# Kernel tuning notes

Hardware: AMD Instinct MI355X
Metric: run time of the kernel (lower is better)

The kernel has to match this reference:

```python
import jax, jax.numpy as jnp
import numpy as np

B, S, D = 2, 2048, 1024
H, DH = 16, 64
N_CTX = 2048
IGNORE = -100000.0


def setup_inputs() -> dict:
    key = jax.random.key(0)
    ks = jax.random.split(key, 6)
    scale = 0.02
    return {
        "x": jax.random.normal(ks[0], (B, S, D), dtype=jnp.float32),
        "W_Q": jax.random.normal(ks[1], (H, DH, D), dtype=jnp.float32) * scale,
        "W_K": jax.random.normal(ks[2], (H, DH, D), dtype=jnp.float32) * scale,
        "W_V": jax.random.normal(ks[3], (H, DH, D), dtype=jnp.float32) * scale,
        "W_O": jax.random.normal(ks[4], (H, D, DH), dtype=jnp.float32) * scale,
        "b_Q": jnp.zeros((H, DH), dtype=jnp.float32),
        "b_K": jnp.zeros((H, DH), dtype=jnp.float32),
        "b_V": jnp.zeros((H, DH), dtype=jnp.float32),
        "b_O": jnp.zeros((D,), dtype=jnp.float32),
    }


def reference(x, W_Q, W_K, W_V, W_O, b_Q, b_K, b_V, b_O):
    attn_scale = jnp.sqrt(jnp.asarray(DH, dtype=x.dtype))
    # q,k,v: [batch, pos, head, d_head]
    q = jnp.einsum('ihm,bpm->bpih', W_Q, x) + b_Q
    k = jnp.einsum('ihm,bpm->bpih', W_K, x) + b_K
    v = jnp.einsum('ihm,bpm->bpih', W_V, x) + b_V
    # scores: [batch, head, q_pos, k_pos]
    attn_scores = jnp.einsum('bpih,bqih->bipq', q, k) / attn_scale
    # causal mask (pos_start=0, no kv cache)
    qs, ks_ = attn_scores.shape[-2], attn_scores.shape[-1]
    mask = jnp.tril(jnp.ones((qs, ks_), dtype=bool))
    attn_scores = jnp.where(mask, attn_scores, jnp.asarray(IGNORE, dtype=attn_scores.dtype))
    attn_matrix = jax.nn.softmax(attn_scores, axis=-1)
    # z: [batch, q_pos, head, d_head]
    z = jnp.einsum('bpih,biqp->bqih', v, attn_matrix)
    out = jnp.einsum('idh,bqih->bqd', W_O, z) + b_O
    return out
```

## Files before the change

### kernel.cpp

```cpp
#include <hip/hip_runtime.h>

typedef __bf16 bf16;
typedef __bf16 bf16x4 __attribute__((ext_vector_type(4)));
typedef __bf16 bf16x8 __attribute__((ext_vector_type(8)));
typedef float f32x4 __attribute__((ext_vector_type(4)));
typedef unsigned u32x4 __attribute__((ext_vector_type(4)));
typedef unsigned u32x2 __attribute__((ext_vector_type(2)));

#define AS1C(p) ((const __attribute__((address_space(1))) void*)(p))
#define AS3(p)  ((__attribute__((address_space(3))) void*)(p))

__device__ __forceinline__ void gld16(const bf16* gsrc, bf16* ldst) {
  __builtin_amdgcn_global_load_lds(AS1C(gsrc), AS3(ldst), 16, 0, 0);
}

#define QSCALE 0.18033688011112042f

__global__ void prep_all(const float* __restrict__ x,
                         const float* __restrict__ WQ, const float* __restrict__ WK,
                         const float* __restrict__ WV, const float* __restrict__ WO,
                         const float* __restrict__ bQ, const float* __restrict__ bK,
                         const float* __restrict__ bV,
                         bf16* __restrict__ xb, bf16* __restrict__ Wqkv,
                         bf16* __restrict__ Wo2, float* __restrict__ biasq) {
  const int X4 = (4096 * 1024) / 4;
  const int WN = 1024 * 1024;
  const int total = X4 + 4 * WN + 3072;
  for (int i = blockIdx.x * blockDim.x + threadIdx.x; i < total; i += gridDim.x * blockDim.x) {
    if (i < X4) {
      float4 v = ((const float4*)x)[i];
      bf16x4 o;
      o[0] = (bf16)v.x; o[1] = (bf16)v.y; o[2] = (bf16)v.z; o[3] = (bf16)v.w;
      ((bf16x4*)xb)[i] = o;
    } else {
      int j = i - X4;
      if (j < WN) {
        Wqkv[j] = (bf16)(WQ[j] * QSCALE);
      } else if (j < 2 * WN) {
        Wqkv[j] = (bf16)WK[j - WN];
      } else if (j < 3 * WN) {
        Wqkv[j] = (bf16)WV[j - 2 * WN];
      } else if (j < 4 * WN) {
        int k = j - 3 * WN;
        int hh = k >> 16, r = k & 65535, d = r >> 6, dh = r & 63;
        Wo2[d * 1024 + hh * 64 + dh] = (bf16)WO[k];
      } else {
        int n = j - 4 * WN;
        biasq[n] = (n < 1024) ? bQ[n] * QSCALE : (n < 2048) ? bK[n - 1024] : bV[n - 2048];
      }
    }
  }
}

template <int MODE>
__global__ __launch_bounds__(256, 2)
void gemm_bt(const bf16* __restrict__ A, const bf16* __restrict__ Bw,
             const float* __restrict__ bias,
             bf16* __restrict__ Qo, bf16* __restrict__ Ko, bf16* __restrict__ Vt,
             float* __restrict__ Co, int M, int N, int K) {
  __shared__ bf16 As[2][8192];
  __shared__ bf16 Bs[2][8192];
  const int tid = threadIdx.x;
  const int lane = tid & 63, w = tid >> 6;
  const int wr = w >> 1, wc = w & 1;
  const int g = lane >> 4, lr = lane & 15;
  const int perx = gridDim.x >> 3;
  const int tile = (blockIdx.x & 7) * perx + (blockIdx.x >> 3);
  const int brow = (tile & 31) * 128, bcol = (tile >> 5) * 128;

  auto stage = [&](int k0, int bufi) {
#pragma unroll
    for (int it = 0; it < 4; ++it) {
      const int cb = (it * 4 + w) * 64;
      const int u = cb + lane;
      const int lc = u ^ ((u >> 3) & 7);
      const int row = lc >> 3, c8 = (lc & 7) * 8;
      gld16(A + (size_t)(brow + row) * K + k0 + c8, &As[bufi][cb * 8]);
      gld16(Bw + (size_t)(bcol + row) * K + k0 + c8, &Bs[bufi][cb * 8]);
    }
  };

  f32x4 acc[4][4] = {};
  stage(0, 0);
  const int nstep = K >> 6;

  for (int t = 0; t < nstep; ++t) {
    __syncthreads();
    if (t + 1 < nstep) stage((t + 1) << 6, (t + 1) & 1);
    const bf16* as = As[t & 1];
    const bf16* bs = Bs[t & 1];
#pragma unroll
    for (int kk = 0; kk < 2; ++kk) {
      bf16x8 af[4], bfm[4];
#pragma unroll
      for (int m = 0; m < 4; ++m) {
        const int row = wr * 64 + m * 16 + lr;
        const int sl = (row * 8 + kk * 4 + g) ^ (lr & 7);
        af[m] = *(const bf16x8*)(as + sl * 8);
      }
#pragma unroll
      for (int n = 0; n < 4; ++n) {
        const int row = wc * 64 + n * 16 + lr;
        const int sl = (row * 8 + kk * 4 + g) ^ (lr & 7);
        bfm[n] = *(const bf16x8*)(bs + sl * 8);
      }
#pragma unroll
      for (int m = 0; m < 4; ++m)
#pragma unroll
        for (int n = 0; n < 4; ++n)
          acc[m][n] = __builtin_amdgcn_mfma_f32_16x16x32_bf16(af[m], bfm[n], acc[m][n], 0, 0, 0);
    }
  }

  const int row0 = brow + wr * 64;
  const int col0 = bcol + wc * 64;
#pragma unroll
  for (int m = 0; m < 4; ++m) {
#pragma unroll
    for (int n = 0; n < 4; ++n) {
      const int nidx = col0 + n * 16 + lr;
      f32x4 v = acc[m][n];
      const float bs = bias[nidx];
      if (MODE == 0) {
        const int stream = nidx >> 10;
        const int j = nidx & 1023;
        const int hh = j >> 6, dh = j & 63;
        const int r0 = row0 + m * 16 + g * 4;
        const int b = r0 >> 11;
        const int p0 = r0 & 2047;
        if (stream == 2) {
          bf16x4 vv;
#pragma unroll
          for (int i = 0; i < 4; ++i) vv[i] = (bf16)(v[i] + bs);
          *(bf16x4*)(Vt + ((size_t)(b * 16 + hh) * 64 + dh) * 2048 + p0) = vv;
        } else {
          bf16* dst = (stream == 0) ? Qo : Ko;
#pragma unroll
          for (int i = 0; i < 4; ++i)
            dst[((size_t)(b * 16 + hh) * 2048 + (p0 + i)) * 64 + dh] = (bf16)(v[i] + bs);
        }
      } else {
#pragma unroll
        for (int i = 0; i < 4; ++i) {
          const int r = row0 + m * 16 + g * 4 + i;
          Co[(size_t)r * 1024 + nidx] = v[i] + bs;
        }
      }
    }
  }
}

__global__ __launch_bounds__(256, 4)
void attn_kernel(const bf16* __restrict__ Qm, const bf16* __restrict__ Km,
                 const bf16* __restrict__ Vm, bf16* __restrict__ Z,
                 bf16* __restrict__ OP, float2* __restrict__ ML) {
  const int nblk = blockIdx.x;
  const int xcd = nblk & 7, s2 = nblk >> 3;
  const int Gl = s2 & 3, u = s2 >> 2;
  const int G = Gl * 8 + xcd;
  const int hh = G & 15, b = G >> 4;
  const int lane = threadIdx.x & 63, w = threadIdx.x >> 6;
  const int g = lane >> 4, lr = lane & 15;
  const bool g0 = g & 1, g1 = (g >> 1) & 1;

  int qt, t0, t1, spl;
  if (u < 32) {
    qt = 31 - (u >> 1); spl = u & 1;
    const int T = qt + 1, mid = (T + 1) >> 1;
    t0 = spl ? mid : 0; t1 = spl ? T : mid;
  } else {
    qt = 47 - u; spl = -1; t0 = 0; t1 = qt + 1;
  }

  __shared__ bf16 Ks[2][4096];
  __shared__ bf16 Vs[2][4096];

  const bf16* Qb = Qm + (size_t)G * 2048 * 64;
  const bf16* Kb = Km + (size_t)G * 2048 * 64;
  const bf16* Vb = Vm + (size_t)G * 64 * 2048;

  auto stage = [&](int kv0, int bufi) {
#pragma unroll
    for (int it = 0; it < 2; ++it) {
      const int cb = w * 128 + it * 64;
      const int uu = cb + lane;
      const int lc = uu ^ ((uu >> 3) & 7);
      const int row = lc >> 3, c8 = (lc & 7) * 8;
      gld16(Kb + (size_t)(kv0 + row) * 64 + c8, &Ks[bufi][cb * 8]);
      gld16(Vb + (size_t)row * 2048 + kv0 + c8, &Vs[bufi][cb * 8]);
    }
  };

  const int q0w = qt * 64 + w * 16;
  const int qg = q0w + lr;

  bf16x8 aq[2];
#pragma unroll
  for (int kk = 0; kk < 2; ++kk)
    aq[kk] = *(const bf16x8*)(Qb + (size_t)qg * 64 + kk * 32 + g * 8);

  float m_i = -1e30f, l_i = 0.f;
  f32x4 oacc[4] = {};

  int buf = 0;
  stage(t0 * 64, 0);
  __syncthreads();

  for (int t = t0; t < t1; ++t) {
    if (t + 1 < t1) stage((t + 1) * 64, buf ^ 1);
    const int kv0 = t * 64;

    f32x4 s[4] = {};
#pragma unroll
    for (int kk = 0; kk < 2; ++kk) {
#pragma unroll
      for (int n = 0; n < 4; ++n) {
        const int r = n * 16 + lr;
        const int sl = (r * 8 + kk * 4 + g) ^ (r & 7);
        bf16x8 bk = *(const bf16x8*)(&Ks[buf][sl * 8]);
        s[n] = __builtin_amdgcn_mfma_f32_16x16x32_bf16(bk, aq[kk], s[n], 0, 0, 0);
      }
    }
    if (t == qt) {
#pragma unroll
      for (int n = 0; n < 4; ++n)
#pragma unroll
        for (int i = 0; i < 4; ++i)
          if (kv0 + n * 16 + g * 4 + i > qg) s[n][i] = -1e9f;
    }

    float tm = fmaxf(fmaxf(fmaxf(s[0][0], s[0][1]), fmaxf(s[0][2], s[0][3])),
                     fmaxf(fmaxf(s[1][0], s[1][1]), fmaxf(s[1][2], s[1][3])));
    tm = fmaxf(tm, fmaxf(fmaxf(fmaxf(s[2][0], s[2][1]), fmaxf(s[2][2], s[2][3])),
                         fmaxf(fmaxf(s[3][0], s[3][1]), fmaxf(s[3][2], s[3][3]))));
    tm = fmaxf(tm, __shfl_xor(tm, 16));
    tm = fmaxf(tm, __shfl_xor(tm, 32));
    if (!__all(tm <= m_i + 12.f)) {
      const float mn = fmaxf(m_i, tm);
      const float al = exp2f(m_i - mn);
      m_i = mn;
      l_i *= al;
#pragma unroll
      for (int n = 0; n < 4; ++n)
#pragma unroll
        for (int i = 0; i < 4; ++i) oacc[n][i] *= al;
    }
#pragma unroll
    for (int n = 0; n < 4; ++n)
#pragma unroll
      for (int i = 0; i < 4; ++i) s[n][i] = exp2f(s[n][i] - m_i);
    float ts = ((s[0][0] + s[0][1]) + (s[0][2] + s[0][3])) +
               ((s[1][0] + s[1][1]) + (s[1][2] + s[1][3])) +
               ((s[2][0] + s[2][1]) + (s[2][2] + s[2][3])) +
               ((s[3][0] + s[3][1]) + (s[3][2] + s[3][3]));
    ts += __shfl_xor(ts, 16);
    ts += __shfl_xor(ts, 32);
    l_i += ts;

    unsigned U[8];
#pragma unroll
    for (int n = 0; n < 4; ++n)
#pragma unroll
      for (int h = 0; h < 2; ++h) {
        unsigned lo = (unsigned)__builtin_bit_cast(unsigned short, (bf16)s[n][2 * h]);
        unsigned hi = (unsigned)__builtin_bit_cast(unsigned short, (bf16)s[n][2 * h + 1]);
        U[n * 2 + h] = lo | (hi << 16);
      }
    unsigned v2_000, v2_001, v2_010, v2_011, v2_100, v2_101, v2_110, v2_111;
#if __has_builtin(__builtin_amdgcn_permlane32_swap)
    {
      u32x2 pA0 = __builtin_amdgcn_permlane32_swap(U[0], U[2], false, false);
      u32x2 pA1 = __builtin_amdgcn_permlane32_swap(U[1], U[3], false, false);
      u32x2 pA2 = __builtin_amdgcn_permlane32_swap(U[4], U[6], false, false);
      u32x2 pA3 = __builtin_amdgcn_permlane32_swap(U[5], U[7], false, false);
      v2_000 = pA0[0]; v2_010 = pA0[1];
      v2_001 = pA1[0]; v2_011 = pA1[1];
      v2_100 = pA2[0]; v2_110 = pA2[1];
      v2_101 = pA3[0]; v2_111 = pA3[1];
    }
#else
    {
      unsigned rA0 = (unsigned)__shfl_xor((int)(g1 ? U[0] : U[2]), 32);
      unsigned rA1 = (unsigned)__shfl_xor((int)(g1 ? U[1] : U[3]), 32);
      unsigned rA2 = (unsigned)__shfl_xor((int)(g1 ? U[4] : U[6]), 32);
      unsigned rA3 = (unsigned)__shfl_xor((int)(g1 ? U[5] : U[7]), 32);
      v2_000 = g1 ? rA0 : U[0];
      v2_001 = g1 ? rA1 : U[1];
      v2_010 = g1 ? U[2] : rA0;
      v2_011 = g1 ? U[3] : rA1;
      v2_100 = g1 ? rA2 : U[4];
      v2_101 = g1 ? rA3 : U[5];
      v2_110 = g1 ? U[6] : rA2;
      v2_111 = g1 ? U[7] : rA3;
    }
#endif
    u32x4 t0v, t1v;
#if __has_builtin(__builtin_amdgcn_permlane16_swap)
    {
      u32x2 pB0 = __builtin_amdgcn_permlane16_swap(v2_000, v2_010, false, false);
      u32x2 pB1 = __builtin_amdgcn_permlane16_swap(v2_001, v2_011, false, false);
      u32x2 pB2 = __builtin_amdgcn_permlane16_swap(v2_100, v2_110, false, false);
      u32x2 pB3 = __builtin_amdgcn_permlane16_swap(v2_101, v2_111, false, false);
      t0v[0] = pB0[0]; t0v[2] = pB0[1];
      t0v[1] = pB1[0]; t0v[3] = pB1[1];
      t1v[0] = pB2[0]; t1v[2] = pB2[1];
      t1v[1] = pB3[0]; t1v[3] = pB3[1];
    }
#else
    {
      unsigned rB0 = (unsigned)__shfl_xor((int)(g0 ? v2_000 : v2_010), 16);
      unsigned rB1 = (unsigned)__shfl_xor((int)(g0 ? v2_001 : v2_011), 16);
      unsigned rB2 = (unsigned)__shfl_xor((int)(g0 ? v2_100 : v2_110), 16);
      unsigned rB3 = (unsigned)__shfl_xor((int)(g0 ? v2_101 : v2_111), 16);
      t0v[0] = g0 ? rB0 : v2_000;
      t0v[1] = g0 ? rB1 : v2_001;
      t0v[2] = g0 ? v2_010 : rB0;
      t0v[3] = g0 ? v2_011 : rB1;
      t1v[0] = g0 ? rB2 : v2_100;
      t1v[1] = g0 ? rB3 : v2_101;
      t1v[2] = g0 ? v2_110 : rB2;
      t1v[3] = g0 ? v2_111 : rB3;
    }
#endif
    bf16x8 pb0 = __builtin_bit_cast(bf16x8, t0v);
    bf16x8 pb1 = __builtin_bit_cast(bf16x8, t1v);

#pragma unroll
    for (int kk = 0; kk < 2; ++kk) {
      const bf16x8 pb = kk ? pb1 : pb0;
#pragma unroll
      for (int n = 0; n < 4; ++n) {
        const int r = n * 16 + lr;
        const int sl = (r * 8 + kk * 4 + g) ^ (r & 7);
        bf16x8 av = *(const bf16x8*)(&Vs[buf][sl * 8]);
        oacc[n] = __builtin_amdgcn_mfma_f32_16x16x32_bf16(av, pb, oacc[n], 0, 0, 0);
      }
    }
    __syncthreads();
    buf ^= 1;
  }

  if (u < 32) {
    const int pr = G * 1024 + (qt - 16) * 64 + w * 16 + lr;
    bf16* oprow = OP + (size_t)(spl * 32768 + pr) * 64;
#pragma unroll
    for (int n = 0; n < 4; ++n) {
      bf16x4 o4;
#pragma unroll
      for (int i = 0; i < 4; ++i) o4[i] = (bf16)oacc[n][i];
      *(bf16x4*)(oprow + n * 16 + g * 4) = o4;
    }
    if (lane < 16) ML[spl * 32768 + pr] = make_float2(m_i, l_i);
  } else {
    const float li = 1.f / l_i;
    bf16* zrow = Z + ((size_t)(b * 2048 + qg) * 16 + hh) * 64;
#pragma unroll
    for (int n = 0; n < 4; ++n) {
      bf16x4 o4;
#pragma unroll
      for (int i = 0; i < 4; ++i) o4[i] = (bf16)(oacc[n][i] * li);
      *(bf16x4*)(zrow + n * 16 + g * 4) = o4;
    }
  }
}

__global__ __launch_bounds__(256)
void combine_kernel(const bf16* __restrict__ OP, const float2* __restrict__ ML,
                    bf16* __restrict__ Z) {
  const int id = blockIdx.x * 256 + threadIdx.x;
  const int pr = id >> 3, d8 = id & 7;
  const float2 ml0 = ML[pr], ml1 = ML[32768 + pr];
  const float m = fmaxf(ml0.x, ml1.x);
  const float w0 = exp2f(ml0.x - m), w1 = exp2f(ml1.x - m);
  const float inv = 1.f / (ml0.y * w0 + ml1.y * w1);
  const bf16x8 a = *(const bf16x8*)(OP + (size_t)pr * 64 + d8 * 8);
  const bf16x8 c = *(const bf16x8*)(OP + ((size_t)32768 + pr) * 64 + d8 * 8);
  bf16x8 o;
#pragma unroll
  for (int j = 0; j < 8; ++j)
    o[j] = (bf16)(((float)a[j] * w0 + (float)c[j] * w1) * inv);
  const int bh = pr >> 10, qr = pr & 1023;
  const int bb = bh >> 4, hq = bh & 15;
  *(bf16x8*)(Z + (((size_t)(bb * 2048 + 1024 + qr)) * 16 + hq) * 64 + d8 * 8) = o;
}

extern "C" void kernel_launch(void* const* d_in, const int* in_sizes, int n_in,
                              void* d_out, int out_size, void* d_ws, size_t ws_size,
                              hipStream_t stream) {
  const float* x  = (const float*)d_in[0];
  const float* WQ = (const float*)d_in[1];
  const float* WK = (const float*)d_in[2];
  const float* WV = (const float*)d_in[3];
  const float* WO = (const float*)d_in[4];
  const float* bQ = (const float*)d_in[5];
  const float* bK = (const float*)d_in[6];
  const float* bV = (const float*)d_in[7];
  const float* bO = (const float*)d_in[8];
  float* out = (float*)d_out;

  char* ws = (char*)d_ws;
  bf16* xb    = (bf16*)(ws);
  bf16* Wqkv  = (bf16*)(ws + (8u << 20));
  bf16* Wo2   = (bf16*)(ws + (14u << 20));
  bf16* Qb    = (bf16*)(ws + (16u << 20));
  bf16* Kb    = (bf16*)(ws + (24u << 20));
  bf16* Vtb   = (bf16*)(ws + (32u << 20));
  bf16* Zb    = (bf16*)(ws + (40u << 20));
  float* biasq = (float*)(ws + (48u << 20));
  bf16* OP    = (bf16*)(ws);
  float2* ML  = (float2*)(ws + (8u << 20));

  prep_all<<<2048, 256, 0, stream>>>(x, WQ, WK, WV, WO, bQ, bK, bV, xb, Wqkv, Wo2, biasq);
  gemm_bt<0><<<768, 256, 0, stream>>>(xb, Wqkv, biasq, Qb, Kb, Vtb, nullptr,
                                      4096, 3072, 1024);
  attn_kernel<<<1536, 256, 0, stream>>>(Qb, Kb, Vtb, Zb, OP, ML);
  combine_kernel<<<1024, 256, 0, stream>>>(OP, ML, Zb);
  gemm_bt<1><<<256, 256, 0, stream>>>(Zb, Wo2, bO, nullptr, nullptr, nullptr, out,
                                      4096, 1024, 1024);
}
```

Before: 205.8 us.

## Process two 64-row query chunks per attention block to reuse K/V tiles

Each attention block now handles 128 query rows as two 64-row chunks that share every staged K/V tile in LDS. This halves K/V global loads and LDS staging per query, and halves the grid from 1536 to 768 blocks with the split and work-order scheme adjusted. In exchange, register use roughly doubles for accumulators and scores, so the occupancy hint drops from 4 to 3 blocks per CU. Diagonal masking now covers two KV tiles per block, so the upper chunk does some fully masked work.

```diff
diff --git a/kernel.cpp b/kernel.cpp
--- a/kernel.cpp
+++ b/kernel.cpp
@@ -150,7 +150,7 @@
   }
 }
 
-__global__ __launch_bounds__(256, 4)
+__global__ __launch_bounds__(256, 3)
 void attn_kernel(const bf16* __restrict__ Qm, const bf16* __restrict__ Km,
                  const bf16* __restrict__ Vm, bf16* __restrict__ Z,
                  bf16* __restrict__ OP, float2* __restrict__ ML) {
@@ -162,14 +162,16 @@
   const int lane = threadIdx.x & 63, w = threadIdx.x >> 6;
   const int g = lane >> 4, lr = lane & 15;
   const bool g0 = g & 1, g1 = (g >> 1) & 1;
-
-  int qt, t0, t1, spl;
-  if (u < 32) {
-    qt = 31 - (u >> 1); spl = u & 1;
-    const int T = qt + 1, mid = (T + 1) >> 1;
-    t0 = spl ? mid : 0; t1 = spl ? T : mid;
+  (void)g0; (void)g1;
+
+  int jt, t0, t1, spl;
+  if (u < 16) {
+    jt = 15 - (u >> 1); spl = u & 1;
+    const int mid = jt + 1;
+    t0 = spl ? mid : 0;
+    t1 = spl ? 2 * jt + 2 : mid;
   } else {
-    qt = 47 - u; spl = -1; t0 = 0; t1 = qt + 1;
+    jt = 23 - u; spl = -1; t0 = 0; t1 = 2 * jt + 2;
   }
 
   __shared__ bf16 Ks[2][4096];
@@ -191,16 +193,17 @@
     }
   };
 
-  const int q0w = qt * 64 + w * 16;
-  const int qg = q0w + lr;
-
-  bf16x8 aq[2];
-#pragma unroll
-  for (int kk = 0; kk < 2; ++kk)
-    aq[kk] = *(const bf16x8*)(Qb + (size_t)qg * 64 + kk * 32 + g * 8);
-
-  float m_i = -1e30f, l_i = 0.f;
-  f32x4 oacc[4] = {};
+  const int qr0 = jt * 128 + w * 16 + lr;
+
+  bf16x8 aq[2][2];
+#pragma unroll
+  for (int c = 0; c < 2; ++c)
+#pragma unroll
+    for (int kk = 0; kk < 2; ++kk)
+      aq[c][kk] = *(const bf16x8*)(Qb + (size_t)(qr0 + c * 64) * 64 + kk * 32 + g * 8);
+
+  float m_i[2] = {-1e30f, -1e30f}, l_i[2] = {0.f, 0.f};
+  f32x4 oacc[2][4] = {};
 
   int buf = 0;
   stage(t0 * 64, 0);
@@ -209,8 +212,9 @@
   for (int t = t0; t < t1; ++t) {
     if (t + 1 < t1) stage((t + 1) * 64, buf ^ 1);
     const int kv0 = t * 64;
-
-    f32x4 s[4] = {};
+    const bool diag = (t >= 2 * jt);
+
+    f32x4 s[2][4] = {};
 #pragma unroll
     for (int kk = 0; kk < 2; ++kk) {
 #pragma unroll
@@ -218,148 +222,166 @@
         const int r = n * 16 + lr;
         const int sl = (r * 8 + kk * 4 + g) ^ (r & 7);
         bf16x8 bk = *(const bf16x8*)(&Ks[buf][sl * 8]);
-        s[n] = __builtin_amdgcn_mfma_f32_16x16x32_bf16(bk, aq[kk], s[n], 0, 0, 0);
-      }
-    }
-    if (t == qt) {
+        s[0][n] = __builtin_amdgcn_mfma_f32_16x16x32_bf16(bk, aq[0][kk], s[0][n], 0, 0, 0);
+        s[1][n] = __builtin_amdgcn_mfma_f32_16x16x32_bf16(bk, aq[1][kk], s[1][n], 0, 0, 0);
+      }
+    }
+    if (diag) {
+#pragma unroll
+      for (int c = 0; c < 2; ++c) {
+        const int qg = qr0 + c * 64;
+#pragma unroll
+        for (int n = 0; n < 4; ++n)
+#pragma unroll
+          for (int i = 0; i < 4; ++i)
+            if (kv0 + n * 16 + g * 4 + i > qg) s[c][n][i] = -1e9f;
+      }
+    }
+
+    bf16x8 pb[2][2];
+#pragma unroll
+    for (int c = 0; c < 2; ++c) {
+      float tm = fmaxf(fmaxf(fmaxf(s[c][0][0], s[c][0][1]), fmaxf(s[c][0][2], s[c][0][3])),
+                       fmaxf(fmaxf(s[c][1][0], s[c][1][1]), fmaxf(s[c][1][2], s[c][1][3])));
+      tm = fmaxf(tm, fmaxf(fmaxf(fmaxf(s[c][2][0], s[c][2][1]), fmaxf(s[c][2][2], s[c][2][3])),
+                           fmaxf(fmaxf(s[c][3][0], s[c][3][1]), fmaxf(s[c][3][2], s[c][3][3]))));
+      tm = fmaxf(tm, __shfl_xor(tm, 16));
+      tm = fmaxf(tm, __shfl_xor(tm, 32));
+      if (!__all(tm <= m_i[c] + 12.f)) {
+        const float mn = fmaxf(m_i[c], tm);
+        const float al = exp2f(m_i[c] - mn);
+        m_i[c] = mn;
+        l_i[c] *= al;
+#pragma unroll
+        for (int n = 0; n < 4; ++n)
+#pragma unroll
+          for (int i = 0; i < 4; ++i) oacc[c][n][i] *= al;
+      }
 #pragma unroll
       for (int n = 0; n < 4; ++n)
 #pragma unroll
-        for (int i = 0; i < 4; ++i)
-          if (kv0 + n * 16 + g * 4 + i > qg) s[n][i] = -1e9f;
-    }
-
-    float tm = fmaxf(fmaxf(fmaxf(s[0][0], s[0][1]), fmaxf(s[0][2], s[0][3])),
-                     fmaxf(fmaxf(s[1][0], s[1][1]), fmaxf(s[1][2], s[1][3])));
-    tm = fmaxf(tm, fmaxf(fmaxf(fmaxf(s[2][0], s[2][1]), fmaxf(s[2][2], s[2][3])),
-                         fmaxf(fmaxf(s[3][0], s[3][1]), fmaxf(s[3][2], s[3][3]))));
-    tm = fmaxf(tm, __shfl_xor(tm, 16));
-    tm = fmaxf(tm, __shfl_xor(tm, 32));
-    if (!__all(tm <= m_i + 12.f)) {
-      const float mn = fmaxf(m_i, tm);
-      const float al = exp2f(m_i - mn);
-      m_i = mn;
-      l_i *= al;
+        for (int i = 0; i < 4; ++i) s[c][n][i] = exp2f(s[c][n][i] - m_i[c]);
+      float ts = ((s[c][0][0] + s[c][0][1]) + (s[c][0][2] + s[c][0][3])) +
+                 ((s[c][1][0] + s[c][1][1]) + (s[c][1][2] + s[c][1][3])) +
+                 ((s[c][2][0] + s[c][2][1]) + (s[c][2][2] + s[c][2][3])) +
+                 ((s[c][3][0] + s[c][3][1]) + (s[c][3][2] + s[c][3][3]));
+      ts += __shfl_xor(ts, 16);
+      ts += __shfl_xor(ts, 32);
+      l_i[c] += ts;
+
+      unsigned U[8];
 #pragma unroll
       for (int n = 0; n < 4; ++n)
 #pragma unroll
-        for (int i = 0; i < 4; ++i) oacc[n][i] *= al;
-    }
-#pragma unroll
-    for (int n = 0; n < 4; ++n)
-#pragma unroll
-      for (int i = 0; i < 4; ++i) s[n][i] = exp2f(s[n][i] - m_i);
-    float ts = ((s[0][0] + s[0][1]) + (s[0][2] + s[0][3])) +
-               ((s[1][0] + s[1][1]) + (s[1][2] + s[1][3])) +
-               ((s[2][0] + s[2][1]) + (s[2][2] + s[2][3])) +
-               ((s[3][0] + s[3][1]) + (s[3][2] + s[3][3]));
-    ts += __shfl_xor(ts, 16);
-    ts += __shfl_xor(ts, 32);
-    l_i += ts;
-
-    unsigned U[8];
-#pragma unroll
-    for (int n = 0; n < 4; ++n)
-#pragma unroll
-      for (int h = 0; h < 2; ++h) {
-        unsigned lo = (unsigned)__builtin_bit_cast(unsigned short, (bf16)s[n][2 * h]);
-        unsigned hi = (unsigned)__builtin_bit_cast(unsigned short, (bf16)s[n][2 * h + 1]);
-        U[n * 2 + h] = lo | (hi << 16);
-      }
-    unsigned v2_000, v2_001, v2_010, v2_011, v2_100, v2_101, v2_110, v2_111;
+        for (int h = 0; h < 2; ++h) {
+          unsigned lo = (unsigned)__builtin_bit_cast(unsigned short, (bf16)s[c][n][2 * h]);
+          unsigned hi = (unsigned)__builtin_bit_cast(unsigned short, (bf16)s[c][n][2 * h + 1]);
+          U[n * 2 + h] = lo | (hi << 16);
+        }
+      unsigned v2_000, v2_001, v2_010, v2_011, v2_100, v2_101, v2_110, v2_111;
 #if __has_builtin(__builtin_amdgcn_permlane32_swap)
-    {
-      u32x2 pA0 = __builtin_amdgcn_permlane32_swap(U[0], U[2], false, false);
-      u32x2 pA1 = __builtin_amdgcn_permlane32_swap(U[1], U[3], false, false);
-      u32x2 pA2 = __builtin_amdgcn_permlane32_swap(U[4], U[6], false, false);
-      u32x2 pA3 = __builtin_amdgcn_permlane32_swap(U[5], U[7], false, false);
-      v2_000 = pA0[0]; v2_010 = pA0[1];
-      v2_001 = pA1[0]; v2_011 = pA1[1];
-      v2_100 = pA2[0]; v2_110 = pA2[1];
-      v2_101 = pA3[0]; v2_111 = pA3[1];
-    }
+      {
+        u32x2 pA0 = __builtin_amdgcn_permlane32_swap(U[0], U[2], false, false);
+        u32x2 pA1 = __builtin_amdgcn_permlane32_swap(U[1], U[3], false, false);
+        u32x2 pA2 = __builtin_amdgcn_permlane32_swap(U[4], U[6], false, false);
+        u32x2 pA3 = __builtin_amdgcn_permlane32_swap(U[5], U[7], false, false);
+        v2_000 = pA0[0]; v2_010 = pA0[1];
+        v2_001 = pA1[0]; v2_011 = pA1[1];
+        v2_100 = pA2[0]; v2_110 = pA2[1];
+        v2_101 = pA3[0]; v2_111 = pA3[1];
+      }
 #else
-    {
-      unsigned rA0 = (unsigned)__shfl_xor((int)(g1 ? U[0] : U[2]), 32);
-      unsigned rA1 = (unsigned)__shfl_xor((int)(g1 ? U[1] : U[3]), 32);
-      unsigned rA2 = (unsigned)__shfl_xor((int)(g1 ? U[4] : U[6]), 32);
-      unsigned rA3 = (unsigned)__shfl_xor((int)(g1 ? U[5] : U[7]), 32);
-      v2_000 = g1 ? rA0 : U[0];
-      v2_001 = g1 ? rA1 : U[1];
-      v2_010 = g1 ? U[2] : rA0;
-      v2_011 = g1 ? U[3] : rA1;
-      v2_100 = g1 ? rA2 : U[4];
-      v2_101 = g1 ? rA3 : U[5];
-      v2_110 = g1 ? U[6] : rA2;
-      v2_111 = g1 ? U[7] : rA3;
-    }
+      {
+        const bool G1 = (lane >> 5) & 1;
+        unsigned rA0 = (unsigned)__shfl_xor((int)(G1 ? U[0] : U[2]), 32);
+        unsigned rA1 = (unsigned)__shfl_xor((int)(G1 ? U[1] : U[3]), 32);
+        unsigned rA2 = (unsigned)__shfl_xor((int)(G1 ? U[4] : U[6]), 32);
+        unsigned rA3 = (unsigned)__shfl_xor((int)(G1 ? U[5] : U[7]), 32);
+        v2_000 = G1 ? rA0 : U[0];
+        v2_001 = G1 ? rA1 : U[1];
+        v2_010 = G1 ? U[2] : rA0;
+        v2_011 = G1 ? U[3] : rA1;
+        v2_100 = G1 ? rA2 : U[4];
+        v2_101 = G1 ? rA3 : U[5];
+        v2_110 = G1 ? U[6] : rA2;
+        v2_111 = G1 ? U[7] : rA3;
+      }
 #endif
-    u32x4 t0v, t1v;
+      u32x4 t0v, t1v;
 #if __has_builtin(__builtin_amdgcn_permlane16_swap)
-    {
-      u32x2 pB0 = __builtin_amdgcn_permlane16_swap(v2_000, v2_010, false, false);
-      u32x2 pB1 = __builtin_amdgcn_permlane16_swap(v2_001, v2_011, false, false);
-      u32x2 pB2 = __builtin_amdgcn_permlane16_swap(v2_100, v2_110, false, false);
-      u32x2 pB3 = __builtin_amdgcn_permlane16_swap(v2_101, v2_111, false, false);
-      t0v[0] = pB0[0]; t0v[2] = pB0[1];
-      t0v[1] = pB1[0]; t0v[3] = pB1[1];
-      t1v[0] = pB2[0]; t1v[2] = pB2[1];
-      t1v[1] = pB3[0]; t1v[3] = pB3[1];
-    }
+      {
+        u32x2 pB0 = __builtin_amdgcn_permlane16_swap(v2_000, v2_010, false, false);
+        u32x2 pB1 = __builtin_amdgcn_permlane16_swap(v2_001, v2_011, false, false);
+        u32x2 pB2 = __builtin_amdgcn_permlane16_swap(v2_100, v2_110, false, false);
+        u32x2 pB3 = __builtin_amdgcn_permlane16_swap(v2_101, v2_111, false, false);
+        t0v[0] = pB0[0]; t0v[2] = pB0[1];
+        t0v[1] = pB1[0]; t0v[3] = pB1[1];
+        t1v[0] = pB2[0]; t1v[2] = pB2[1];
+        t1v[1] = pB3[0]; t1v[3] = pB3[1];
+      }
 #else
-    {
-      unsigned rB0 = (unsigned)__shfl_xor((int)(g0 ? v2_000 : v2_010), 16);
-      unsigned rB1 = (unsigned)__shfl_xor((int)(g0 ? v2_001 : v2_011), 16);
-      unsigned rB2 = (unsigned)__shfl_xor((int)(g0 ? v2_100 : v2_110), 16);
-      unsigned rB3 = (unsigned)__shfl_xor((int)(g0 ? v2_101 : v2_111), 16);
-      t0v[0] = g0 ? rB0 : v2_000;
-      t0v[1] = g0 ? rB1 : v2_001;
-      t0v[2] = g0 ? v2_010 : rB0;
-      t0v[3] = g0 ? v2_011 : rB1;
-      t1v[0] = g0 ? rB2 : v2_100;
-      t1v[1] = g0 ? rB3 : v2_101;
-      t1v[2] = g0 ? v2_110 : rB2;
-      t1v[3] = g0 ? v2_111 : rB3;
-    }
+      {
+        const bool G0 = (lane >> 4) & 1;
+        unsigned rB0 = (unsigned)__shfl_xor((int)(G0 ? v2_000 : v2_010), 16);
+        unsigned rB1 = (unsigned)__shfl_xor((int)(G0 ? v2_001 : v2_011), 16);
+        unsigned rB2 = (unsigned)__shfl_xor((int)(G0 ? v2_100 : v2_110), 16);
+        unsigned rB3 = (unsigned)__shfl_xor((int)(G0 ? v2_101 : v2_111), 16);
+        t0v[0] = G0 ? rB0 : v2_000;
+        t0v[1] = G0 ? rB1 : v2_001;
+        t0v[2] = G0 ? v2_010 : rB0;
+        t0v[3] = G0 ? v2_011 : rB1;
+        t1v[0] = G0 ? rB2 : v2_100;
+        t1v[1] = G0 ? rB3 : v2_101;
+        t1v[2] = G0 ? v2_110 : rB2;
+        t1v[3] = G0 ? v2_111 : rB3;
+      }
 #endif
-    bf16x8 pb0 = __builtin_bit_cast(bf16x8, t0v);
-    bf16x8 pb1 = __builtin_bit_cast(bf16x8, t1v);
+      pb[c][0] = __builtin_bit_cast(bf16x8, t0v);
+      pb[c][1] = __builtin_bit_cast(bf16x8, t1v);
+    }
 
 #pragma unroll
     for (int kk = 0; kk < 2; ++kk) {
-      const bf16x8 pb = kk ? pb1 : pb0;
 #pragma unroll
       for (int n = 0; n < 4; ++n) {
         const int r = n * 16 + lr;
         const int sl = (r * 8 + kk * 4 + g) ^ (r & 7);
         bf16x8 av = *(const bf16x8*)(&Vs[buf][sl * 8]);
-        oacc[n] = __builtin_amdgcn_mfma_f32_16x16x32_bf16(av, pb, oacc[n], 0, 0, 0);
+        oacc[0][n] = __builtin_amdgcn_mfma_f32_16x16x32_bf16(av, pb[0][kk], oacc[0][n], 0, 0, 0);
+        oacc[1][n] = __builtin_amdgcn_mfma_f32_16x16x32_bf16(av, pb[1][kk], oacc[1][n], 0, 0, 0);
       }
     }
     __syncthreads();
     buf ^= 1;
   }
 
-  if (u < 32) {
-    const int pr = G * 1024 + (qt - 16) * 64 + w * 16 + lr;
-    bf16* oprow = OP + (size_t)(spl * 32768 + pr) * 64;
-#pragma unroll
-    for (int n = 0; n < 4; ++n) {
-      bf16x4 o4;
-#pragma unroll
-      for (int i = 0; i < 4; ++i) o4[i] = (bf16)oacc[n][i];
-      *(bf16x4*)(oprow + n * 16 + g * 4) = o4;
-    }
-    if (lane < 16) ML[spl * 32768 + pr] = make_float2(m_i, l_i);
+  if (u < 16) {
+#pragma unroll
+    for (int c = 0; c < 2; ++c) {
+      const int pr = G * 1024 + (jt - 8) * 128 + c * 64 + w * 16 + lr;
+      bf16* oprow = OP + (size_t)(spl * 32768 + pr) * 64;
+#pragma unroll
+      for (int n = 0; n < 4; ++n) {
+        bf16x4 o4;
+#pragma unroll
+        for (int i = 0; i < 4; ++i) o4[i] = (bf16)oacc[c][n][i];
+        *(bf16x4*)(oprow + n * 16 + g * 4) = o4;
+      }
+      if (lane < 16) ML[spl * 32768 + pr] = make_float2(m_i[c], l_i[c]);
+    }
   } else {
-    const float li = 1.f / l_i;
-    bf16* zrow = Z + ((size_t)(b * 2048 + qg) * 16 + hh) * 64;
-#pragma unroll
-    for (int n = 0; n < 4; ++n) {
-      bf16x4 o4;
-#pragma unroll
-      for (int i = 0; i < 4; ++i) o4[i] = (bf16)(oacc[n][i] * li);
-      *(bf16x4*)(zrow + n * 16 + g * 4) = o4;
+#pragma unroll
+    for (int c = 0; c < 2; ++c) {
+      const float li = 1.f / l_i[c];
+      const int qg = qr0 + c * 64;
+      bf16* zrow = Z + ((size_t)(b * 2048 + qg) * 16 + hh) * 64;
+#pragma unroll
+      for (int n = 0; n < 4; ++n) {
+        bf16x4 o4;
+#pragma unroll
+        for (int i = 0; i < 4; ++i) o4[i] = (bf16)(oacc[c][n][i] * li);
+        *(bf16x4*)(zrow + n * 16 + g * 4) = o4;
+      }
     }
   }
 }
@@ -413,7 +435,7 @@
   prep_all<<<2048, 256, 0, stream>>>(x, WQ, WK, WV, WO, bQ, bK, bV, xb, Wqkv, Wo2, biasq);
   gemm_bt<0><<<768, 256, 0, stream>>>(xb, Wqkv, biasq, Qb, Kb, Vtb, nullptr,
                                       4096, 3072, 1024);
-  attn_kernel<<<1536, 256, 0, stream>>>(Qb, Kb, Vtb, Zb, OP, ML);
+  attn_kernel<<<768, 256, 0, stream>>>(Qb, Kb, Vtb, Zb, OP, ML);
   combine_kernel<<<1024, 256, 0, stream>>>(OP, ML, Zb);
   gemm_bt<1><<<256, 256, 0, stream>>>(Zb, Wo2, bO, nullptr, nullptr, nullptr, out,
                                       4096, 1024, 1024);
```

Result: slower. 214.9 us (+4.4%).
